# Kernel tuning notes

Measured on AMD Instinct MI355X. Metric: run time of the kernel, lower is better.

## Reference

```python
import jax, jax.numpy as jnp
import numpy as np
from jax import lax

EPS = 1e-5
B, NV, NP, C = 1, 12000, 32, 5
VF = 128            # voxel_feat_dim
OF = 256            # output_feat_dim
D0, H0, W0 = 16, 128, 128


def _bn(x, gamma, beta, axes):
    # training-mode batch norm (biased variance), channel dim broadcasts via gamma/beta shape
    mean = jnp.mean(x, axis=axes, keepdims=True)
    var = jnp.var(x, axis=axes, keepdims=True)
    return (x - mean) * lax.rsqrt(var + EPS) * gamma + beta


def _vfe(x, w, b, gamma, beta):
    # x: (B, NVox, NPts, Cin) -> (B, NVox, Cout); linear -> BN1d over all rows -> relu -> max over points
    y = jnp.einsum('bvpc,co->bvpo', x, w) + b
    Bv, Nv, Pp, Co = y.shape
    y = _bn(y.reshape(Bv * Nv * Pp, Co), gamma, beta, axes=0).reshape(Bv, Nv, Pp, Co)
    y = jax.nn.relu(y)
    return jnp.max(y, axis=2)


def _conv_bn_relu(x, w, b, gamma, beta):
    y = lax.conv_general_dilated(x, w, (2, 2, 2), [(1, 1)] * 3,
                                 dimension_numbers=('NCDHW', 'OIDHW', 'NCDHW'))
    y = y + b[None, :, None, None, None]
    y = _bn(y, gamma[None, :, None, None, None], beta[None, :, None, None, None], axes=(0, 2, 3, 4))
    return jax.nn.relu(y)


def setup_inputs() -> dict:
    key = jax.random.key(0)
    ks = jax.random.split(key, 20)
    vf = VF // 2
    inp = {
        'voxel_features': jax.random.normal(ks[0], (B, NV, NP, C), jnp.float32),
        'voxel_coords': jnp.stack([
            jax.random.randint(ks[1], (B, NV), 0, D0),
            jax.random.randint(ks[2], (B, NV), 0, H0),
            jax.random.randint(ks[3], (B, NV), 0, W0)], axis=-1).astype(jnp.int32),
        'grid_d': D0, 'grid_h': H0, 'grid_w': W0,
        # VFE1: 5 -> 64
        'w1': jax.random.normal(ks[4], (C, vf), jnp.float32) * 0.05,
        'b1': jnp.zeros((vf,), jnp.float32),
        'g1': jnp.ones((vf,), jnp.float32),
        'be1': jnp.zeros((vf,), jnp.float32),
        # VFE2: 64 -> 128
        'w2': jax.random.normal(ks[5], (vf, VF), jnp.float32) * 0.05,
        'b2': jnp.zeros((VF,), jnp.float32),
        'g2': jnp.ones((VF,), jnp.float32),
        'be2': jnp.zeros((VF,), jnp.float32),
        # conv3d stack
        'cw1': jax.random.normal(ks[6], (128, VF, 3, 3, 3), jnp.float32) * 0.02,
        'cb1': jnp.zeros((128,), jnp.float32),
        'cg1': jnp.ones((128,), jnp.float32),
        'cbe1': jnp.zeros((128,), jnp.float32),
        'cw2': jax.random.normal(ks[7], (256, 128, 3, 3, 3), jnp.float32) * 0.02,
        'cb2': jnp.zeros((256,), jnp.float32),
        'cg2': jnp.ones((256,), jnp.float32),
        'cbe2': jnp.zeros((256,), jnp.float32),
        'cw3': jax.random.normal(ks[8], (OF, 256, 3, 3, 3), jnp.float32) * 0.02,
        'cb3': jnp.zeros((OF,), jnp.float32),
        'cg3': jnp.ones((OF,), jnp.float32),
        'cbe3': jnp.zeros((OF,), jnp.float32),
    }
    return inp


def reference(voxel_features, voxel_coords, grid_d, grid_h, grid_w,
              w1, b1, g1, be1, w2, b2, g2, be2,
              cw1, cb1, cg1, cbe1, cw2, cb2, cg2, cbe2, cw3, cb3, cg3, cbe3):
    # VFE1: (B, NV, NP, C) -> (B, NV, 64)
    f = _vfe(voxel_features, w1, b1, g1, be1)
    # VFE2 (repaired: singleton points dim, max over 1 point is identity)
    f = _vfe(f[:, :, None, :], w2, b2, g2, be2)  # (B, NV, 128)

    Bn, Nn, Cf = f.shape
    grid = jnp.zeros((Bn, grid_d, grid_h, grid_w, Cf), f.dtype)
    bidx = jnp.broadcast_to(jnp.arange(Bn)[:, None], (Bn, Nn))
    grid = grid.at[bidx, voxel_coords[..., 0], voxel_coords[..., 1], voxel_coords[..., 2]].set(f)
    grid = jnp.transpose(grid, (0, 4, 1, 2, 3))  # (B, Cf, D, H, W)

    x = _conv_bn_relu(grid, cw1, cb1, cg1, cbe1)
    x = _conv_bn_relu(x, cw2, cb2, cg2, cbe2)
    x = _conv_bn_relu(x, cw3, cb3, cg3, cbe3)
    return x
```

## Files before the change

### kernel.cpp

```cpp
#include <hip/hip_runtime.h>

#define NVOX 12000
#define NPTS 32
#define CIN  5
#define C1   64
#define C2   128
#define GD   16
#define GH   128
#define GW   128
#define SP   (GD*GH*GW)
static constexpr float EPSBN = 1e-5f;

typedef unsigned short ushortT;
typedef __attribute__((ext_vector_type(8))) short bf16x8;
typedef __attribute__((ext_vector_type(4))) float f32x4;

__device__ inline ushortT f2bf(float f) {
    unsigned int x = __float_as_uint(f);
    unsigned int r = (x + 0x7FFFu + ((x >> 16) & 1u)) >> 16;
    return (ushortT)r;
}
__device__ inline float bf2f(ushortT u) { return __uint_as_float(((unsigned int)u) << 16); }

__device__ inline void gload16(const ushortT* g, ushortT* l) {
    __builtin_amdgcn_global_load_lds(
        (const __attribute__((address_space(1))) unsigned int*)g,
        (__attribute__((address_space(3))) unsigned int*)l, 16, 0, 0);
}

#define P1D 18
#define P1H 130
#define P1W 130
#define PSP1 (P1D*P1H*P1W)
#define P2D 10
#define P2H 66
#define P2W 66
#define PSP2 (P2D*P2H*P2W)
#define P3D 6
#define P3H 34
#define P3W 34
#define PSP3 (P3D*P3H*P3W)


__device__ inline void conv_w_one(const float* cw, ushortT* wb, int CI_, int TCO_,
                                  int NS_, int e) {
    int j = e & 7;
    int rest = e >> 3;
    int CHN = TCO_*16;
    int p = rest % CHN; int r = rest / CHN;
    int s = r % NS_;    int cob = r / NS_;
    int col = p >> 4, cp = p & 15;
    int cl = cp ^ (col & 7);
    int tap = (CI_==256) ? (s>>1) : s;
    int cib = (CI_==256) ? ((s&1)*128) : 0;
    int co = cob*TCO_ + col;
    int ci = cib + cl*8 + j;
    wb[e] = f2bf(cw[((size_t)co*CI_ + ci)*27 + tap]);
}

__global__ void prep(const float* __restrict__ x, const float* __restrict__ w1,
                     float* __restrict__ s1sum,
                     const float* __restrict__ cw1, const float* __restrict__ cw2,
                     const float* __restrict__ cw3, ushortT* __restrict__ wb1,
                     ushortT* __restrict__ wb2, ushortT* __restrict__ wb3,
                     const int* __restrict__ coords, int* __restrict__ winner) {
    __shared__ float s_w[CIN*C1];
    __shared__ float s_red[2][4][C1];
    const int blk = blockIdx.x;
    const int t = threadIdx.x;
    if (blk < 960) {
        for (int i = t; i < CIN*C1; i += 256) s_w[i] = w1[i];
        __syncthreads();
        int ch = t & 63, rr = t >> 6;
        float sum = 0.f, sq = 0.f;
        const int NROWS = NVOX * NPTS;
        for (int row = blk*4 + rr; row < NROWS; row += 960*4) {
            const float* xr = x + row*CIN;
            float y = 0.f;
            #pragma unroll
            for (int c = 0; c < CIN; ++c) y += xr[c] * s_w[c*C1 + ch];
            sum += y; sq += y*y;
        }
        s_red[0][rr][ch] = sum; s_red[1][rr][ch] = sq;
        __syncthreads();
        if (rr == 0) {
            sum = s_red[0][0][ch]+s_red[0][1][ch]+s_red[0][2][ch]+s_red[0][3][ch];
            sq  = s_red[1][0][ch]+s_red[1][1][ch]+s_red[1][2][ch]+s_red[1][3][ch];
            atomicAdd(&s1sum[ch], sum);
            atomicAdd(&s1sum[C1+ch], sq);
        }
    } else if (blk < 1984) {
        const int N1 = 442368, N2 = 884736, N3 = 1769472;
        const int total = N1+N2+N3;
        for (int e0 = (blk-960)*256 + t; e0 < total; e0 += 1024*256) {
            if (e0 < N1)         conv_w_one(cw1, wb1, 128, 128, 27, e0);
            else if (e0 < N1+N2) conv_w_one(cw2, wb2, 128, 64,  27, e0-N1);
            else                 conv_w_one(cw3, wb3, 256, 64,  54, e0-N1-N2);
        }
    } else {
        int v = (blk-1984)*256 + t;
        if (v < NVOX) {
            int d = coords[v*3+0], h = coords[v*3+1], w = coords[v*3+2];
            atomicMax(&winner[(d*GH + h)*GW + w], v);
        }
    }
}

__global__ void vfe1_apply(const float* __restrict__ x, const float* __restrict__ w1,
                           const float* __restrict__ sums, const float* __restrict__ g,
                           const float* __restrict__ be, float* __restrict__ f1) {
    __shared__ float s_w[CIN*C1];
    __shared__ float s_x[4*NPTS*CIN];
    int v0 = blockIdx.x*4, t = threadIdx.x;
    for (int i = t; i < CIN*C1; i += 256) s_w[i] = w1[i];
    for (int i = t; i < 4*NPTS*CIN; i += 256) s_x[i] = x[(size_t)v0*NPTS*CIN + i];
    int sub = t >> 6, ch = t & 63;
    const float invN = 1.f/(NVOX*NPTS);
    float mean = sums[ch]*invN;
    float var  = sums[C1+ch]*invN - mean*mean;
    float sc = g[ch]*rsqrtf(var + EPSBN);
    float sh = be[ch] - mean*sc;
    __syncthreads();
    float m = 0.f;
    const float* xs = s_x + sub*NPTS*CIN;
    for (int p = 0; p < NPTS; ++p) {
        float y = 0.f;
        #pragma unroll
        for (int c = 0; c < CIN; ++c) y += xs[p*CIN+c]*s_w[c*C1+ch];
        m = fmaxf(m, y*sc + sh);
    }
    f1[(v0+sub)*C1 + ch] = m;
}

__global__ void vfe2_linear(const float* __restrict__ f1, const float* __restrict__ w2,
                            float* __restrict__ y2, float* __restrict__ sums) {
    __shared__ float s_w[C2][68];
    __shared__ float s_f[16*C1];
    int t = threadIdx.x;
    for (int i = t; i < C1*C2; i += 128) {
        int c = i >> 7, o = i & 127;
        s_w[o][c] = w2[i];
    }
    int v0 = blockIdx.x*16;
    for (int i = t; i < 16*C1; i += 128) s_f[i] = f1[v0*C1 + i];
    __syncthreads();
    float sum = 0.f, sq = 0.f;
    for (int vl = 0; vl < 16; ++vl) {
        float y = 0.f;
        #pragma unroll
        for (int c4 = 0; c4 < C1; c4 += 4) {
            float4 f = *(const float4*)&s_f[vl*C1 + c4];
            float4 w = *(const float4*)&s_w[t][c4];
            y += f.x*w.x + f.y*w.y + f.z*w.z + f.w*w.w;
        }
        y2[(v0+vl)*C2 + t] = y;
        sum += y; sq += y*y;
    }
    atomicAdd(&sums[t], sum);
    atomicAdd(&sums[C2+t], sq);
}

__global__ void vfe2_apply_bf16(const float* __restrict__ y2, const float* __restrict__ sums,
                                const float* __restrict__ g, const float* __restrict__ be,
                                ushortT* __restrict__ f2b) {
    __shared__ float s_sc[C2], s_sh[C2];
    int t = threadIdx.x;
    if (t < C2) {
        const float invN = 1.f/NVOX;
        float mean = sums[t]*invN;
        float var  = sums[C2+t]*invN - mean*mean;
        float sc = g[t]*rsqrtf(var + EPSBN);
        s_sc[t] = sc; s_sh[t] = be[t] - mean*sc;
    }
    __syncthreads();
    int i = blockIdx.x*256 + t;
    if (i >= NVOX*C2/4) return;
    const float4 v = *(const float4*)(y2 + (size_t)i*4);
    int c0 = (i*4) & (C2-1);
    ushort4 o;
    o.x = f2bf(fmaxf(0.f, v.x*s_sc[c0+0]+s_sh[c0+0]));
    o.y = f2bf(fmaxf(0.f, v.y*s_sc[c0+1]+s_sh[c0+1]));
    o.z = f2bf(fmaxf(0.f, v.z*s_sc[c0+2]+s_sh[c0+2]));
    o.w = f2bf(fmaxf(0.f, v.w*s_sc[c0+3]+s_sh[c0+3]));
    *(ushort4*)(f2b + (size_t)i*4) = o;
}

__global__ void build_grid_cl(const int* __restrict__ winner, const ushortT* __restrict__ f2b,
                              ushortT* __restrict__ grid) {
    const int total = PSP1*16;
    for (int e = blockIdx.x*256 + threadIdx.x; e < total; e += gridDim.x*256) {
        int pos = e >> 4, ch = e & 15;
        int pz = pos / (P1H*P1W); int rr = pos % (P1H*P1W);
        int py = rr / P1W; int px = rr % P1W;
        unsigned dz = pz-1, dy = py-1, dx = px-1;
        int4 v = {0,0,0,0};
        if (dz < GD && dy < GH && dx < GW) {
            int wn_ = winner[(dz*GH + dy)*GW + dx];
            if (wn_ >= 0) v = *(const int4*)(f2b + (size_t)wn_*C2 + ch*8);
        }
        *(int4*)(grid + ((size_t)pos << 7) + ch*8) = v;
    }
}

template<int CI, int CO, int TILE_CO, int TILE_SP, int THREADS,
         int WAVES_M, int WAVES_N,
         int PD, int PH, int PW, int DO, int HO, int WO,
         int OPH, int OPW, int NS, int NSLICE, bool ATOMIC>
__global__ __launch_bounds__(THREADS) void conv3d_mfma(
        const ushortT* __restrict__ in_p, const ushortT* __restrict__ wb,
        void* __restrict__ outp, float* __restrict__ sums_out) {
    constexpr int FRAG_M = TILE_CO/(WAVES_M*16);
    constexpr int FRAG_N = TILE_SP/(WAVES_N*16);
    constexpr int TILE_Y = TILE_SP/8;
    constexpr int SPB    = NS/NSLICE;
    constexpr int WTAP   = TILE_CO*128;
    constexpr int XCH    = TILE_SP*16/THREADS;
    constexpr int WCHN   = TILE_CO*16/THREADS;

    __shared__ ushortT s_x[2][TILE_SP*128];
    __shared__ ushortT s_w[2][TILE_CO*128];

    constexpr int nbx = WO/8, nby = HO/TILE_Y;
    constexpr int NWG = nbx*nby*DO*(CO/TILE_CO)*NSLICE;
    int b = (blockIdx.x & 7)*(NWG >> 3) + (blockIdx.x >> 3);
    const int bx = b % nbx; b /= nbx;
    const int by = b % nby; b /= nby;
    const int bz = b % DO;  b /= DO;
    const int cob   = b % (CO/TILE_CO);
    const int slice = b / (CO/TILE_CO);
    const int co0 = cob*TILE_CO;
    const int oy0 = by*TILE_Y, ox0 = bx*8;
    const int t = threadIdx.x;
    const int lane = t & 63, wid = t >> 6;
    const int lr = lane & 15, lq = lane >> 4;
    const int wm = wid % WAVES_M, wn = wid / WAVES_M;

    size_t xpre[XCH];
    #pragma unroll
    for (int j = 0; j < XCH; ++j) {
        int q = t + j*THREADS;
        int n = q >> 4, cp = q & 15;
        int cl = cp ^ (n & 7);
        int oy = n >> 3, ox = n & 7;
        xpre[j] = (size_t)(((2*bz)*PH + (2*oy0 + 2*oy))*PW + (2*ox0 + 2*ox))*CI + cl*8;
    }
    int aoff[FRAG_M], axr[FRAG_M], boff[FRAG_N], bxr[FRAG_N];
    #pragma unroll
    for (int f = 0; f < FRAG_M; ++f) {
        int c = wm*(FRAG_M*16) + f*16 + lr;
        aoff[f] = c*128; axr[f] = c & 7;
    }
    #pragma unroll
    for (int f = 0; f < FRAG_N; ++f) {
        int n = wn*(FRAG_N*16) + f*16 + lr;
        boff[f] = n*128; bxr[f] = n & 7;
    }

    f32x4 acc[FRAG_M][FRAG_N];
    #pragma unroll
    for (int i = 0; i < FRAG_M; ++i)
        #pragma unroll
        for (int j = 0; j < FRAG_N; ++j) acc[i][j] = (f32x4){0.f,0.f,0.f,0.f};

    const int s0 = slice*SPB;

#define STAGE(bufi, s) { \
    const int tap_ = (CI==256) ? ((s)>>1) : (s); \
    const int cib_ = (CI==256) ? (((s)&1)*128) : 0; \
    const int kz_ = tap_/9, ky_ = (tap_/3)%3, kx_ = tap_%3; \
    const ushortT* wsrc_ = wb + ((size_t)(cob*NS + (s)))*WTAP; \
    _Pragma("unroll") for (int j = 0; j < WCHN; ++j) \
        gload16(wsrc_ + (size_t)(t + j*THREADS)*8, &s_w[bufi][(wid*64 + j*THREADS)*8]); \
    const size_t koff_ = (size_t)((kz_*PH + ky_)*PW + kx_)*CI + cib_; \
    _Pragma("unroll") for (int j = 0; j < XCH; ++j) \
        gload16(in_p + xpre[j] + koff_, &s_x[bufi][(wid*64 + j*THREADS)*8]); }

#define COMPUTE(bufi) { \
    _Pragma("unroll") for (int ks = 0; ks < 4; ++ks) { \
        int cl_ = ks*4 + lq; \
        bf16x8 av[FRAG_M], bv[FRAG_N]; \
        _Pragma("unroll") for (int f = 0; f < FRAG_M; ++f) \
            av[f] = *(const bf16x8*)&s_w[bufi][aoff[f] + ((cl_ ^ axr[f])<<3)]; \
        _Pragma("unroll") for (int f = 0; f < FRAG_N; ++f) \
            bv[f] = *(const bf16x8*)&s_x[bufi][boff[f] + ((cl_ ^ bxr[f])<<3)]; \
        _Pragma("unroll") for (int i = 0; i < FRAG_M; ++i) \
        _Pragma("unroll") for (int j = 0; j < FRAG_N; ++j) \
            acc[i][j] = __builtin_amdgcn_mfma_f32_16x16x32_bf16(av[i], bv[j], acc[i][j],0,0,0); } }

    STAGE(0, s0);
    __syncthreads();
    #pragma unroll
    for (int ph = 0; ph < SPB; ++ph) {
        const int buf = ph & 1;
        if (ph + 1 < SPB) STAGE(buf^1, s0 + ph + 1);
        COMPUTE(buf);
        __syncthreads();
    }
#undef STAGE
#undef COMPUTE

    if constexpr (!ATOMIC) {
        ushortT* out = (ushortT*)outp;
        #pragma unroll
        for (int fm = 0; fm < FRAG_M; ++fm)
        #pragma unroll
        for (int fn = 0; fn < FRAG_N; ++fn) {
            int n = wn*(FRAG_N*16) + fn*16 + lr;
            int oy = n >> 3, ox = n & 7;
            int c_ = co0 + wm*(FRAG_M*16) + fm*16 + lq*4;
            size_t pa = ((size_t)(bz+1)*OPH + (oy0+oy+1))*OPW + (ox0+ox+1);
            ushort4 o;
            o.x = f2bf(acc[fm][fn][0]); o.y = f2bf(acc[fm][fn][1]);
            o.z = f2bf(acc[fm][fn][2]); o.w = f2bf(acc[fm][fn][3]);
            *(ushort4*)(out + pa*CO + c_) = o;
        }
        #pragma unroll
        for (int fm = 0; fm < FRAG_M; ++fm) {
            float sv[4], qv[4];
            #pragma unroll
            for (int r = 0; r < 4; ++r) {
                float ssum = 0.f, qsum = 0.f;
                #pragma unroll
                for (int fn = 0; fn < FRAG_N; ++fn) {
                    float a = acc[fm][fn][r]; ssum += a; qsum += a*a;
                }
                #pragma unroll
                for (int m = 1; m < 16; m <<= 1) {
                    ssum += __shfl_xor(ssum, m, 64);
                    qsum += __shfl_xor(qsum, m, 64);
                }
                sv[r] = ssum; qv[r] = qsum;
            }
            if (lr == 0) {
                int c_ = co0 + wm*(FRAG_M*16) + fm*16 + lq*4;
                #pragma unroll
                for (int r = 0; r < 4; ++r) {
                    atomicAdd(&sums_out[c_+r], sv[r]);
                    atomicAdd(&sums_out[CO + c_+r], qv[r]);
                }
            }
        }
    } else {
        float* out = (float*)outp;
        #pragma unroll
        for (int fm = 0; fm < FRAG_M; ++fm)
        #pragma unroll
        for (int fn = 0; fn < FRAG_N; ++fn) {
            int n = wn*(FRAG_N*16) + fn*16 + lr;
            int oy = n >> 3, ox = n & 7;
            int c_ = co0 + wm*(FRAG_M*16) + fm*16 + lq*4;
            #pragma unroll
            for (int r = 0; r < 4; ++r)
                atomicAdd(&out[((size_t)(c_+r)*DO + bz)*(HO*WO) + (oy0+oy)*WO + ox0+ox],
                          acc[fm][fn][r]);
        }
    }
}

template<int C, int PD, int PH, int PW>
__global__ void bn_apply_pad(ushortT* __restrict__ y, const float* __restrict__ sums,
                             const float* __restrict__ g, const float* __restrict__ be,
                             float invN) {
    constexpr int CH = C/8;
    constexpr int total = PD*PH*PW*CH;
    __shared__ float s_sc[C], s_sh[C];
    for (int c = threadIdx.x; c < C; c += 256) {
        float mean = sums[c]*invN;
        float var  = sums[C+c]*invN - mean*mean;
        float sc = g[c]*rsqrtf(var + EPSBN);
        s_sc[c] = sc; s_sh[c] = be[c] - mean*sc;
    }
    __syncthreads();
    for (int e = blockIdx.x*256 + threadIdx.x; e < total; e += gridDim.x*256) {
        int pos = e / CH;
        int c0 = (e % CH)*8;
        int pz = pos / (PH*PW); int rr = pos % (PH*PW);
        int py = rr / PW; int px = rr % PW;
        if ((unsigned)(pz-1) >= (unsigned)(PD-2) || (unsigned)(py-1) >= (unsigned)(PH-2) ||
            (unsigned)(px-1) >= (unsigned)(PW-2)) continue;
        ushortT* p = y + (size_t)pos*C + c0;
        ushort4 a = *(ushort4*)p, b4 = *(ushort4*)(p+4);
        ushort4 o1, o2;
        o1.x = f2bf(fmaxf(0.f, bf2f(a.x)*s_sc[c0+0]+s_sh[c0+0]));
        o1.y = f2bf(fmaxf(0.f, bf2f(a.y)*s_sc[c0+1]+s_sh[c0+1]));
        o1.z = f2bf(fmaxf(0.f, bf2f(a.z)*s_sc[c0+2]+s_sh[c0+2]));
        o1.w = f2bf(fmaxf(0.f, bf2f(a.w)*s_sc[c0+3]+s_sh[c0+3]));
        o2.x = f2bf(fmaxf(0.f, bf2f(b4.x)*s_sc[c0+4]+s_sh[c0+4]));
        o2.y = f2bf(fmaxf(0.f, bf2f(b4.y)*s_sc[c0+5]+s_sh[c0+5]));
        o2.z = f2bf(fmaxf(0.f, bf2f(b4.z)*s_sc[c0+6]+s_sh[c0+6]));
        o2.w = f2bf(fmaxf(0.f, bf2f(b4.w)*s_sc[c0+7]+s_sh[c0+7]));
        *(ushort4*)p     = o1;
        *(ushort4*)(p+4) = o2;
    }
}

template<int SPL>
__global__ void bn_stats_cmajor(const float* __restrict__ y, const float* __restrict__ g,
                                const float* __restrict__ be, float* __restrict__ ss, int C) {
    __shared__ float s_red[2][256];
    int c = blockIdx.x;
    const float* p = y + (size_t)c*SPL;
    float sum = 0.f, sq = 0.f;
    for (int i = threadIdx.x; i < SPL; i += 256) { float v = p[i]; sum += v; sq += v*v; }
    s_red[0][threadIdx.x] = sum; s_red[1][threadIdx.x] = sq;
    __syncthreads();
    for (int s = 128; s > 0; s >>= 1) {
        if (threadIdx.x < s) {
            s_red[0][threadIdx.x] += s_red[0][threadIdx.x+s];
            s_red[1][threadIdx.x] += s_red[1][threadIdx.x+s];
        }
        __syncthreads();
    }
    if (threadIdx.x == 0) {
        float invN = 1.f/(float)SPL;
        float mean = s_red[0][0]*invN;
        float var  = s_red[1][0]*invN - mean*mean;
        float sc = g[c]*rsqrtf(var + EPSBN);
        ss[c] = sc; ss[C+c] = be[c] - mean*sc;
    }
}

template<int LOGSPL>
__global__ void bn_apply_cmajor(float* __restrict__ y, const float* __restrict__ ss,
                                int C, int total) {
    for (int i = blockIdx.x*blockDim.x + threadIdx.x; i < total; i += gridDim.x*blockDim.x) {
        int c = i >> LOGSPL;
        y[i] = fmaxf(0.f, y[i]*ss[c] + ss[C+c]);
    }
}

extern "C" void kernel_launch(void* const* d_in, const int* in_sizes, int n_in,
                              void* d_out, int out_size, void* d_ws, size_t ws_size,
                              hipStream_t stream) {
    const float* x      = (const float*)d_in[0];
    const int*   coords = (const int*)  d_in[1];
    const float* w1  = (const float*)d_in[5];
    const float* g1  = (const float*)d_in[7];
    const float* be1 = (const float*)d_in[8];
    const float* w2  = (const float*)d_in[9];
    const float* g2  = (const float*)d_in[11];
    const float* be2 = (const float*)d_in[12];
    const float* cw1 = (const float*)d_in[13];
    const float* cg1 = (const float*)d_in[15];
    const float* cbe1= (const float*)d_in[16];
    const float* cw2 = (const float*)d_in[17];
    const float* cg2 = (const float*)d_in[19];
    const float* cbe2= (const float*)d_in[20];
    const float* cw3 = (const float*)d_in[21];
    const float* cg3 = (const float*)d_in[23];
    const float* cbe3= (const float*)d_in[24];
    float* out = (float*)d_out;

    float*   ws     = (float*)d_ws;
    float*   stats  = ws;
    int*     winner = (int*)(ws + 4096);
    float*   f1     = (float*)(winner + SP);
    float*   y2     = f1 + (size_t)NVOX*C1;
    ushortT* f2b    = (ushortT*)(y2 + (size_t)NVOX*C2);
    ushortT* grid   = f2b + (size_t)NVOX*C2;
    ushortT* c1o    = grid + (size_t)PSP1*128;
    ushortT* c2o    = c1o + (size_t)PSP2*128;
    ushortT* wb1    = c2o + (size_t)PSP3*256;
    ushortT* wb2    = wb1 + 442368;
    ushortT* wb3    = wb2 + 884736;

    float* s1sum = stats;
    float* s2sum = stats + 128;
    float* c1sum = stats + 384;
    float* c2sum = stats + 640;
    float* ss3   = stats + 1152;

    hipMemsetAsync(stats, 0, 4096*sizeof(float), stream);
    hipMemsetAsync(winner, 0xFF, SP*sizeof(int), stream);
    hipMemsetAsync(c1o, 0, (size_t)PSP2*128*2, stream);
    hipMemsetAsync(c2o, 0, (size_t)PSP3*256*2, stream);
    hipMemsetAsync(d_out, 0, (size_t)out_size*sizeof(float), stream);

    prep<<<2031, 256, 0, stream>>>(x, w1, s1sum, cw1, cw2, cw3, wb1, wb2, wb3,
                                   coords, winner);
    vfe1_apply<<<NVOX/4, 256, 0, stream>>>(x, w1, s1sum, g1, be1, f1);
    vfe2_linear<<<NVOX/16, 128, 0, stream>>>(f1, w2, y2, s2sum);
    vfe2_apply_bf16<<<NVOX*C2/4/256, 256, 0, stream>>>(y2, s2sum, g2, be2, f2b);
    build_grid_cl<<<4096, 256, 0, stream>>>(winner, f2b, grid);

    conv3d_mfma<128,128, 128,128,256, 2,2, P1D,P1H,P1W, 8,64,64, P2H,P2W, 27,1,false>
        <<<8*4*8, 256, 0, stream>>>(grid, wb1, c1o, c1sum);
    bn_apply_pad<128, P2D,P2H,P2W><<<1024, 256, 0, stream>>>(c1o, c1sum, cg1, cbe1,
                                                             1.f/32768.f);
    conv3d_mfma<128,256, 64,64,256, 2,2, P2D,P2H,P2W, 4,32,32, P3H,P3W, 27,1,false>
        <<<4*4*4*4, 256, 0, stream>>>(c1o, wb2, c2o, c2sum);
    bn_apply_pad<256, P3D,P3H,P3W><<<512, 256, 0, stream>>>(c2o, c2sum, cg2, cbe2,
                                                            1.f/4096.f);
    conv3d_mfma<256,256, 64,64,256, 2,2, P3D,P3H,P3W, 2,16,16, 1,1, 54,6,true>
        <<<2*2*2*4*6, 256, 0, stream>>>(c2o, wb3, (void*)out, nullptr);

    bn_stats_cmajor<2*16*16><<<256, 256, 0, stream>>>(out, cg3, cbe3, ss3, 256);
    bn_apply_cmajor<9><<<512, 256, 0, stream>>>(out, ss3, 256, 131072);
}
```

Measured before the change: 306.1 us.

## Triple-buffer conv3d MFMA pipeline with 64-channel K-steps and explicit vmcnt waits

The conv3d MFMA kernel now stages 64 input channels per step instead of 128, which doubles the number of K-steps. The weight prepack layout and its XOR swizzle are changed to match. The LDS ring buffer goes from two to three stages, with loads issued two steps ahead and explicit s_waitcnt vmcnt plus raw s_barrier replacing __syncthreads, so global loads overlap more with MFMA work. The first conv's spatial tile shrinks to 64, doubling its workgroup count, and launch bounds request 3 blocks per CU. The aim is to hide load latency and raise occupancy, at the cost of more barriers per tap and hand-counted vmcnt values that must match the number of outstanding loads.

```diff
diff --git a/kernel.cpp b/kernel.cpp
--- a/kernel.cpp
+++ b/kernel.cpp
@@ -46,15 +46,16 @@
                                   int NS_, int e) {
     int j = e & 7;
     int rest = e >> 3;
-    int CHN = TCO_*16;
+    int CHN = TCO_*8;
     int p = rest % CHN; int r = rest / CHN;
     int s = r % NS_;    int cob = r / NS_;
-    int col = p >> 4, cp = p & 15;
-    int cl = cp ^ (col & 7);
-    int tap = (CI_==256) ? (s>>1) : s;
-    int cib = (CI_==256) ? ((s&1)*128) : 0;
+    int col = p >> 3, slot = p & 7;
+    int logical = slot ^ (col & 7);
+    int nh = CI_ >> 6;
+    int tap = s / nh;
+    int cib = (s % nh) * 64;
     int co = cob*TCO_ + col;
-    int ci = cib + cl*8 + j;
+    int ci = cib + logical*8 + j;
     wb[e] = f2bf(cw[((size_t)co*CI_ + ci)*27 + tap]);
 }
 
@@ -93,9 +94,9 @@
         const int N1 = 442368, N2 = 884736, N3 = 1769472;
         const int total = N1+N2+N3;
         for (int e0 = (blk-960)*256 + t; e0 < total; e0 += 1024*256) {
-            if (e0 < N1)         conv_w_one(cw1, wb1, 128, 128, 27, e0);
-            else if (e0 < N1+N2) conv_w_one(cw2, wb2, 128, 64,  27, e0-N1);
-            else                 conv_w_one(cw3, wb3, 256, 64,  54, e0-N1-N2);
+            if (e0 < N1)         conv_w_one(cw1, wb1, 128, 128, 54, e0);
+            else if (e0 < N1+N2) conv_w_one(cw2, wb2, 128, 64,  54, e0-N1);
+            else                 conv_w_one(cw3, wb3, 256, 64, 108, e0-N1-N2);
         }
     } else {
         int v = (blk-1984)*256 + t;
@@ -202,59 +203,53 @@
     }
 }
 
-template<int CI, int CO, int TILE_CO, int TILE_SP, int THREADS,
-         int WAVES_M, int WAVES_N,
+template<int CI, int CO, int TCO, int TSP, int THREADS, int WM, int WN,
          int PD, int PH, int PW, int DO, int HO, int WO,
          int OPH, int OPW, int NS, int NSLICE, bool ATOMIC>
-__global__ __launch_bounds__(THREADS) void conv3d_mfma(
+__global__ __launch_bounds__(THREADS, 3) void conv3d_mfma(
         const ushortT* __restrict__ in_p, const ushortT* __restrict__ wb,
         void* __restrict__ outp, float* __restrict__ sums_out) {
-    constexpr int FRAG_M = TILE_CO/(WAVES_M*16);
-    constexpr int FRAG_N = TILE_SP/(WAVES_N*16);
-    constexpr int TILE_Y = TILE_SP/8;
+    constexpr int FRAG_M = TCO/(WM*16);
+    constexpr int FRAG_N = TSP/(WN*16);
+    constexpr int TILE_Y = TSP/8;
     constexpr int SPB    = NS/NSLICE;
-    constexpr int WTAP   = TILE_CO*128;
-    constexpr int XCH    = TILE_SP*16/THREADS;
-    constexpr int WCHN   = TILE_CO*16/THREADS;
-
-    __shared__ ushortT s_x[2][TILE_SP*128];
-    __shared__ ushortT s_w[2][TILE_CO*128];
+    constexpr int WCHN   = TCO*8/THREADS;
+    constexpr int XCH    = TSP*8/THREADS;
+    constexpr int CHT    = WCHN + XCH;
+
+    __shared__ ushortT s_x[3][TSP*64];
+    __shared__ ushortT s_w[3][TCO*64];
 
     constexpr int nbx = WO/8, nby = HO/TILE_Y;
-    constexpr int NWG = nbx*nby*DO*(CO/TILE_CO)*NSLICE;
+    constexpr int NWG = nbx*nby*DO*(CO/TCO)*NSLICE;
     int b = (blockIdx.x & 7)*(NWG >> 3) + (blockIdx.x >> 3);
     const int bx = b % nbx; b /= nbx;
     const int by = b % nby; b /= nby;
     const int bz = b % DO;  b /= DO;
-    const int cob   = b % (CO/TILE_CO);
-    const int slice = b / (CO/TILE_CO);
-    const int co0 = cob*TILE_CO;
+    const int cob   = b % (CO/TCO);
+    const int slice = b / (CO/TCO);
+    const int co0 = cob*TCO;
     const int oy0 = by*TILE_Y, ox0 = bx*8;
     const int t = threadIdx.x;
     const int lane = t & 63, wid = t >> 6;
     const int lr = lane & 15, lq = lane >> 4;
-    const int wm = wid % WAVES_M, wn = wid / WAVES_M;
+    const int wm = wid % WM, wn = wid / WM;
 
     size_t xpre[XCH];
     #pragma unroll
     for (int j = 0; j < XCH; ++j) {
         int q = t + j*THREADS;
-        int n = q >> 4, cp = q & 15;
-        int cl = cp ^ (n & 7);
+        int n = q >> 3, slot = q & 7;
+        int cp = slot ^ (n & 7);
         int oy = n >> 3, ox = n & 7;
-        xpre[j] = (size_t)(((2*bz)*PH + (2*oy0 + 2*oy))*PW + (2*ox0 + 2*ox))*CI + cl*8;
-    }
-    int aoff[FRAG_M], axr[FRAG_M], boff[FRAG_N], bxr[FRAG_N];
+        xpre[j] = ((size_t)((2*bz)*PH + 2*(oy0+oy))*PW + 2*(ox0+ox))*CI + cp*8;
+    }
+    const int xr = lr & 7;
+    int aoff[FRAG_M], boff[FRAG_N];
     #pragma unroll
-    for (int f = 0; f < FRAG_M; ++f) {
-        int c = wm*(FRAG_M*16) + f*16 + lr;
-        aoff[f] = c*128; axr[f] = c & 7;
-    }
+    for (int f = 0; f < FRAG_M; ++f) aoff[f] = (wm*(FRAG_M*16) + f*16 + lr)*64;
     #pragma unroll
-    for (int f = 0; f < FRAG_N; ++f) {
-        int n = wn*(FRAG_N*16) + f*16 + lr;
-        boff[f] = n*128; bxr[f] = n & 7;
-    }
+    for (int f = 0; f < FRAG_N; ++f) boff[f] = (wn*(FRAG_N*16) + f*16 + lr)*64;
 
     f32x4 acc[FRAG_M][FRAG_N];
     #pragma unroll
@@ -265,10 +260,10 @@
     const int s0 = slice*SPB;
 
 #define STAGE(bufi, s) { \
-    const int tap_ = (CI==256) ? ((s)>>1) : (s); \
-    const int cib_ = (CI==256) ? (((s)&1)*128) : 0; \
+    const int tap_ = (s) / (CI/64); \
+    const int cib_ = ((s) % (CI/64))*64; \
     const int kz_ = tap_/9, ky_ = (tap_/3)%3, kx_ = tap_%3; \
-    const ushortT* wsrc_ = wb + ((size_t)(cob*NS + (s)))*WTAP; \
+    const ushortT* wsrc_ = wb + ((size_t)(cob*NS + (s)))*(TCO*64); \
     _Pragma("unroll") for (int j = 0; j < WCHN; ++j) \
         gload16(wsrc_ + (size_t)(t + j*THREADS)*8, &s_w[bufi][(wid*64 + j*THREADS)*8]); \
     const size_t koff_ = (size_t)((kz_*PH + ky_)*PW + kx_)*CI + cib_; \
@@ -276,25 +271,35 @@
         gload16(in_p + xpre[j] + koff_, &s_x[bufi][(wid*64 + j*THREADS)*8]); }
 
 #define COMPUTE(bufi) { \
-    _Pragma("unroll") for (int ks = 0; ks < 4; ++ks) { \
-        int cl_ = ks*4 + lq; \
+    _Pragma("unroll") for (int ks = 0; ks < 2; ++ks) { \
+        const int sl_ = ((ks*4 + lq) ^ xr) << 3; \
         bf16x8 av[FRAG_M], bv[FRAG_N]; \
         _Pragma("unroll") for (int f = 0; f < FRAG_M; ++f) \
-            av[f] = *(const bf16x8*)&s_w[bufi][aoff[f] + ((cl_ ^ axr[f])<<3)]; \
+            av[f] = *(const bf16x8*)&s_w[bufi][aoff[f] + sl_]; \
         _Pragma("unroll") for (int f = 0; f < FRAG_N; ++f) \
-            bv[f] = *(const bf16x8*)&s_x[bufi][boff[f] + ((cl_ ^ bxr[f])<<3)]; \
+            bv[f] = *(const bf16x8*)&s_x[bufi][boff[f] + sl_]; \
         _Pragma("unroll") for (int i = 0; i < FRAG_M; ++i) \
         _Pragma("unroll") for (int j = 0; j < FRAG_N; ++j) \
             acc[i][j] = __builtin_amdgcn_mfma_f32_16x16x32_bf16(av[i], bv[j], acc[i][j],0,0,0); } }
 
     STAGE(0, s0);
-    __syncthreads();
+    STAGE(1, s0+1);
     #pragma unroll
     for (int ph = 0; ph < SPB; ++ph) {
-        const int buf = ph & 1;
-        if (ph + 1 < SPB) STAGE(buf^1, s0 + ph + 1);
+        const int buf = ph % 3;
+        if (ph + 2 < SPB) STAGE((ph+2)%3, s0+ph+2);
+        if (ph + 2 < SPB) {
+            asm volatile("s_waitcnt vmcnt(%0)" :: "i"(2*CHT) : "memory");
+        } else if (ph + 1 < SPB) {
+            asm volatile("s_waitcnt vmcnt(%0)" :: "i"(CHT) : "memory");
+        } else {
+            asm volatile("s_waitcnt vmcnt(0)" ::: "memory");
+        }
+        __builtin_amdgcn_s_barrier();
+        __builtin_amdgcn_sched_barrier(0);
         COMPUTE(buf);
-        __syncthreads();
+        __builtin_amdgcn_sched_barrier(0);
+        __builtin_amdgcn_s_barrier();
     }
 #undef STAGE
 #undef COMPUTE
@@ -483,15 +488,15 @@
     vfe2_apply_bf16<<<NVOX*C2/4/256, 256, 0, stream>>>(y2, s2sum, g2, be2, f2b);
     build_grid_cl<<<4096, 256, 0, stream>>>(winner, f2b, grid);
 
-    conv3d_mfma<128,128, 128,128,256, 2,2, P1D,P1H,P1W, 8,64,64, P2H,P2W, 27,1,false>
-        <<<8*4*8, 256, 0, stream>>>(grid, wb1, c1o, c1sum);
+    conv3d_mfma<128,128, 128,64,256, 2,2, P1D,P1H,P1W, 8,64,64, P2H,P2W, 54,1,false>
+        <<<8*8*8, 256, 0, stream>>>(grid, wb1, c1o, c1sum);
     bn_apply_pad<128, P2D,P2H,P2W><<<1024, 256, 0, stream>>>(c1o, c1sum, cg1, cbe1,
                                                              1.f/32768.f);
-    conv3d_mfma<128,256, 64,64,256, 2,2, P2D,P2H,P2W, 4,32,32, P3H,P3W, 27,1,false>
+    conv3d_mfma<128,256, 64,64,256, 2,2, P2D,P2H,P2W, 4,32,32, P3H,P3W, 54,1,false>
         <<<4*4*4*4, 256, 0, stream>>>(c1o, wb2, c2o, c2sum);
     bn_apply_pad<256, P3D,P3H,P3W><<<512, 256, 0, stream>>>(c2o, c2sum, cg2, cbe2,
                                                             1.f/4096.f);
-    conv3d_mfma<256,256, 64,64,256, 2,2, P3D,P3H,P3W, 2,16,16, 1,1, 54,6,true>
+    conv3d_mfma<256,256, 64,64,256, 2,2, P3D,P3H,P3W, 2,16,16, 1,1, 108,6,true>
         <<<2*2*2*4*6, 256, 0, stream>>>(c2o, wb3, (void*)out, nullptr);
 
     bn_stats_cmajor<2*16*16><<<256, 256, 0, stream>>>(out, cg3, cbe3, ss3, 256);
```

Measured after the change: 342.7 us. 11.9% more time.
